# Optimization experiments

Hardware: AMD Instinct MI355X
Metric: run time of the kernel (lower is better)

The kernel has to match this reference:

```python
import jax, jax.numpy as jnp
import numpy as np

B, N, E_PER = 64, 1024, 32768
IN_DIM, HID, K = 128, 128, 64
EPS = 1e-15


def setup_inputs() -> dict:
    key = jax.random.key(0)
    ks = jax.random.split(key, 16)
    x = jax.random.normal(ks[0], (B * N, IN_DIM), jnp.float32)
    off = (jnp.arange(B, dtype=jnp.int32) * N)[:, None]
    src = (jax.random.randint(ks[1], (B, E_PER), 0, N, dtype=jnp.int32) + off).reshape(-1)
    dst = (jax.random.randint(ks[2], (B, E_PER), 0, N, dtype=jnp.int32) + off).reshape(-1)
    edge_index = jnp.stack([src, dst])
    batch = jnp.repeat(jnp.arange(B, dtype=jnp.int32), N)

    def lin(k, i, o):
        return (jax.random.normal(k, (i, o), jnp.float32) / np.sqrt(i)).astype(jnp.float32)

    params = dict(
        W1l=lin(ks[3], IN_DIM, HID), b1l=jnp.zeros((HID,), jnp.float32), W1r=lin(ks[4], IN_DIM, HID),
        W2l=lin(ks[5], HID, K), b2l=jnp.zeros((K,), jnp.float32), W2r=lin(ks[6], HID, K),
        Wm=lin(ks[7], K, K), bm=jnp.zeros((K,), jnp.float32),
        Wrel=lin(ks[8], HID, HID), Wroot=lin(ks[9], HID, HID), broot=jnp.zeros((HID,), jnp.float32),
        Wc1=lin(ks[10], HID * K, HID), bc1=jnp.zeros((HID,), jnp.float32),
        Wc2=lin(ks[11], HID, 1), bc2=jnp.zeros((1,), jnp.float32),
    )
    return dict(x=x, edge_index=edge_index, batch=batch, num_graphs=B, nodes_per_graph=N, **params)


def _sage(x, src, dst, Wl, bl, Wr, n):
    # PyG SAGEConv: lin_l(mean_{j in N(i)} x_j) + lin_r(x_i); lin_r has no bias.
    agg = jax.ops.segment_sum(x[src], dst, num_segments=n)
    deg = jax.ops.segment_sum(jnp.ones((src.shape[0],), x.dtype), dst, num_segments=n)
    agg = agg / jnp.maximum(deg, 1.0)[:, None]
    return agg @ Wl + bl + x @ Wr


def reference(x, edge_index, batch, num_graphs, nodes_per_graph,
              W1l, b1l, W1r, W2l, b2l, W2r, Wm, bm,
              Wrel, Wroot, broot, Wc1, bc1, Wc2, bc2):
    Bn, Nn = num_graphs, nodes_per_graph
    n_total = Bn * Nn
    src, dst = edge_index[0], edge_index[1]

    z = jax.nn.leaky_relu(_sage(x, src, dst, W1l, b1l, W1r, n_total), 0.01)
    s = jax.nn.leaky_relu(_sage(z, src, dst, W2l, b2l, W2r, n_total), 0.01)
    s = s @ Wm + bm

    # to_dense_batch (equal-size graphs -> mask all True) and to_dense_adj
    z = z.reshape(Bn, Nn, -1)                      # [B, N, HID]
    s = s.reshape(Bn, Nn, -1)                      # [B, N, K]
    a = jnp.zeros((Bn, Nn, Nn), x.dtype).at[src // Nn, src % Nn, dst % Nn].add(1.0)

    # dense_diff_pool
    s = jax.nn.softmax(s, axis=-1)
    pooled = jnp.einsum('bnk,bnf->bkf', s, z)      # [B, K, HID]
    adj_p = jnp.einsum('bnk,bnm,bml->bkl', s, a, s)  # [B, K, K]
    link_loss = jnp.sqrt(jnp.sum((a - jnp.einsum('bnk,bmk->bnm', s, s)) ** 2)) / a.size
    ent_loss = jnp.mean(jnp.sum(-s * jnp.log(s + EPS), axis=-1))

    # DenseSAGEConv: lin_rel(adj@x / deg) + lin_root(x)
    agg = jnp.matmul(adj_p, pooled) / jnp.maximum(adj_p.sum(-1, keepdims=True), 1.0)
    h = jax.nn.leaky_relu(agg @ Wrel + pooled @ Wroot + broot, 0.01)

    h = h.reshape(Bn, -1)                          # [B, K*HID]
    logits = (jax.nn.leaky_relu(h @ Wc1 + bc1, 0.01) @ Wc2 + bc2).squeeze(-1)
    return logits, link_loss + ent_loss
```

## Files before the change

### kernel.cpp

```cpp
#include <hip/hip_runtime.h>
#include <math.h>

#define BATCH 64
#define NPG 1024
#define NT (BATCH*NPG)
#define EPER 32768
#define ETOT (BATCH*EPER)

typedef __attribute__((ext_vector_type(4))) float f32x4;
typedef __attribute__((ext_vector_type(8))) short s16x8;

__device__ __forceinline__ float lky(float x){ return x > 0.f ? x : 0.01f*x; }
__device__ __forceinline__ unsigned short f2bf(float f){
    unsigned u = __float_as_uint(f);
    u = u + 0x7FFFu + ((u >> 16) & 1u);
    return (unsigned short)(u >> 16);
}
__device__ __forceinline__ float bf2f_lo(unsigned v){ return __uint_as_float(v << 16); }
__device__ __forceinline__ float bf2f_hi(unsigned v){ return __uint_as_float(v & 0xFFFF0000u); }

__global__ void k_castx(const float* __restrict__ in, unsigned short* __restrict__ out, int n4){
    int i = blockIdx.x*256 + threadIdx.x;
    if (i < n4){
        float4 v = ((const float4*)in)[i];
        ushort4 o = { f2bf(v.x), f2bf(v.y), f2bf(v.z), f2bf(v.w) };
        ((ushort4*)out)[i] = o;
    }
}

__global__ void k_wprep(const float* __restrict__ W1l, const float* __restrict__ W1r,
                        const float* __restrict__ W2l, const float* __restrict__ W2r,
                        unsigned short* __restrict__ wt){
    int i = blockIdx.x*256 + threadIdx.x;
    if (i < 16384){ int k = i >> 7, n = i & 127; wt[n*128 + k] = f2bf(W1l[i]); }
    else if (i < 32768){ int j = i - 16384; int k = j >> 7, n = j & 127; wt[16384 + n*128 + k] = f2bf(W1r[j]); }
    else if (i < 40960){ int j = i - 32768; int k = j >> 6, n = j & 63; wt[32768 + n*128 + k] = f2bf(W2l[j]); }
    else if (i < 49152){ int j = i - 40960; int k = j >> 6, n = j & 63; wt[40960 + n*128 + k] = f2bf(W2r[j]); }
}

__global__ void __launch_bounds__(1024) k_a2lds(const int* __restrict__ src, const int* __restrict__ dst,
                                                unsigned* __restrict__ acc_out){
    __shared__ unsigned nib[32768];
    __shared__ unsigned red[16];
    int b = blockIdx.x, pass = blockIdx.y, tid = threadIdx.x;
    for (int i = tid; i < 32768; i += 1024) nib[i] = 0;
    __syncthreads();
    int base = b*EPER;
    for (int i = tid; i < EPER; i += 1024){
        unsigned key = (((unsigned)src[base+i] & 1023u) << 10) | ((unsigned)dst[base+i] & 1023u);
        if ((int)(key >> 18) == pass)
            atomicAdd(&nib[(key & 0x3FFFFu) >> 3], 1u << ((key & 7u)*4u));
    }
    __syncthreads();
    unsigned local = 0;
    for (int i = tid; i < 32768; i += 1024){
        unsigned w = nib[i];
        if (w){
            #pragma unroll
            for (int q = 0; q < 8; q++){ unsigned c = (w >> (4*q)) & 15u; local += c*c; }
        }
    }
    for (int o = 32; o; o >>= 1) local += __shfl_xor(local, o);
    if ((tid & 63) == 0) red[tid >> 6] = local;
    __syncthreads();
    if (tid == 0){
        unsigned s = 0;
        for (int q = 0; q < 16; q++) s += red[q];
        atomicAdd(acc_out, s);
    }
}

__global__ void __launch_bounds__(1024) k_csr(const int* __restrict__ src, const int* __restrict__ dst,
                                              int* __restrict__ ipd, int* __restrict__ ips,
                                              unsigned short* __restrict__ lst_d,
                                              unsigned short* __restrict__ lst_s){
    __shared__ unsigned eds[EPER];
    __shared__ int cnt[1024];
    __shared__ int buf[1024];
    int g = blockIdx.x, which = blockIdx.y, tid = threadIdx.x;
    cnt[tid] = 0;
    __syncthreads();
    int base = g*EPER;
    for (int i = tid; i < EPER; i += 1024){
        unsigned s = (unsigned)src[base+i] & 1023u;
        unsigned d = (unsigned)dst[base+i] & 1023u;
        eds[i] = (s << 10) | d;
        atomicAdd(&cnt[which ? s : d], 1);
    }
    __syncthreads();
    int v = cnt[tid];
    int x = v;
    buf[tid] = x; __syncthreads();
    for (int off = 1; off < 1024; off <<= 1){
        int t = (tid >= off) ? buf[tid - off] : 0;
        __syncthreads();
        x += t; buf[tid] = x; __syncthreads();
    }
    int excl = x - v;
    int* ip = which ? ips : ipd;
    ip[g*1024 + tid] = base + excl;
    if (g == 0 && tid == 0) ip[NT] = ETOT;
    cnt[tid] = excl;
    __syncthreads();
    unsigned short* lst = which ? lst_s : lst_d;
    for (int i = tid; i < EPER; i += 1024){
        unsigned key = eds[i];
        unsigned d = key & 1023u, s = key >> 10;
        unsigned idx = which ? s : d;
        unsigned val = which ? d : s;
        int p = atomicAdd(&cnt[idx], 1);
        lst[base + p] = (unsigned short)val;
    }
}

template<int MODE, int TD>
__global__ void __launch_bounds__(1024) k_aggl(
        const unsigned short* __restrict__ X, const int* __restrict__ indptr,
        const unsigned short* __restrict__ lst,
        const unsigned short* __restrict__ R, const float* __restrict__ bias,
        unsigned short* __restrict__ out){
    __shared__ uint2 tab[1024*9];
    constexpr int PPG = (TD == 128) ? 8 : 4;
    int bid = blockIdx.x;
    int xcd = bid & 7, j = bid >> 3;
    int gi = j / PPG, part = j - gi*PPG;
    int graph = xcd + 8*gi;
    int fpart = part >> 1;
    int npart = part & 1;
    int foff = fpart*32;
    int nbase_loc = npart*512;
    int tid = threadIdx.x;
    int gb = graph*NPG;
    for (int i = tid; i < 8192; i += 1024){
        int row = i >> 3, q = i & 7;
        tab[row*9 + q] = *(const uint2*)&X[(size_t)(gb+row)*TD + foff + q*4];
    }
    __syncthreads();
    int g = tid & 7;
    for (int c = 0; c < 4; c++){
        int node = gb + nbase_loc + c*128 + (tid >> 3);
        int st = indptr[node], en = indptr[node+1];
        float a0 = 0.f, a1 = 0.f, a2 = 0.f, a3 = 0.f;
        int e = st;
        for (; e + 4 <= en; e += 4){
            int r0 = lst[e+0], r1 = lst[e+1], r2 = lst[e+2], r3 = lst[e+3];
            uint2 v0 = tab[r0*9 + g];
            uint2 v1 = tab[r1*9 + g];
            uint2 v2 = tab[r2*9 + g];
            uint2 v3 = tab[r3*9 + g];
            a0 += bf2f_lo(v0.x) + bf2f_lo(v1.x) + bf2f_lo(v2.x) + bf2f_lo(v3.x);
            a1 += bf2f_hi(v0.x) + bf2f_hi(v1.x) + bf2f_hi(v2.x) + bf2f_hi(v3.x);
            a2 += bf2f_lo(v0.y) + bf2f_lo(v1.y) + bf2f_lo(v2.y) + bf2f_lo(v3.y);
            a3 += bf2f_hi(v0.y) + bf2f_hi(v1.y) + bf2f_hi(v2.y) + bf2f_hi(v3.y);
        }
        for (; e < en; e++){
            uint2 v = tab[lst[e]*9 + g];
            a0 += bf2f_lo(v.x); a1 += bf2f_hi(v.x);
            a2 += bf2f_lo(v.y); a3 += bf2f_hi(v.y);
        }
        if (MODE >= 1){
            int dg = en - st;
            float inv = 1.f/(float)(dg > 1 ? dg : 1);
            a0 *= inv; a1 *= inv; a2 *= inv; a3 *= inv;
        }
        if (MODE == 2){
            uint2 r = *(const uint2*)&R[(size_t)node*TD + foff + 4*g];
            a0 = lky(a0 + bf2f_lo(r.x) + bias[foff + 4*g + 0]);
            a1 = lky(a1 + bf2f_hi(r.x) + bias[foff + 4*g + 1]);
            a2 = lky(a2 + bf2f_lo(r.y) + bias[foff + 4*g + 2]);
            a3 = lky(a3 + bf2f_hi(r.y) + bias[foff + 4*g + 3]);
        }
        uint2 pk;
        pk.x = (unsigned)f2bf(a0) | ((unsigned)f2bf(a1) << 16);
        pk.y = (unsigned)f2bf(a2) | ((unsigned)f2bf(a3) << 16);
        *(uint2*)&out[(size_t)node*TD + foff + 4*g] = pk;
    }
}

template<int N>
__global__ void __launch_bounds__(512) k_mfma2b(
        const unsigned short* __restrict__ Ah, const unsigned short* __restrict__ Wt1,
        const unsigned short* __restrict__ Wt2, unsigned short* __restrict__ C1,
        unsigned short* __restrict__ C2){
    __shared__ unsigned short ldsB[2*N*128];
    int tid = threadIdx.x;
    for (int i = tid; i < N*64; i += 512){
        int n = i >> 6, kk = i & 63;
        int swz = (n*256 + 4*kk) ^ ((n & 7) << 4);
        *(unsigned*)((char*)ldsB + swz)         = ((const unsigned*)Wt1)[i];
        *(unsigned*)((char*)ldsB + N*256 + swz) = ((const unsigned*)Wt2)[i];
    }
    __syncthreads();
    int wave = tid >> 6, l = tid & 63;
    int lr = l & 15, lg = l >> 4;
    constexpr int NF = N/16;
    int arow = blockIdx.x*128 + wave*16 + lr;
    f32x4 acc1[NF], acc2[NF];
    f32x4 zv = {0.f, 0.f, 0.f, 0.f};
    #pragma unroll
    for (int nf = 0; nf < NF; nf++){ acc1[nf] = zv; acc2[nf] = zv; }
    #pragma unroll
    for (int ks = 0; ks < 4; ks++){
        s16x8 af = *(const s16x8*)(Ah + (size_t)arow*128 + ks*32 + lg*8);
        #pragma unroll
        for (int nf = 0; nf < NF; nf++){
            int n = nf*16 + lr;
            int swz = (n*256 + ks*64 + lg*16) ^ ((n & 7) << 4);
            s16x8 b1 = *(const s16x8*)((const char*)ldsB + swz);
            s16x8 b2 = *(const s16x8*)((const char*)ldsB + N*256 + swz);
            acc1[nf] = __builtin_amdgcn_mfma_f32_16x16x32_bf16(af, b1, acc1[nf], 0, 0, 0);
            acc2[nf] = __builtin_amdgcn_mfma_f32_16x16x32_bf16(af, b2, acc2[nf], 0, 0, 0);
        }
    }
    int orow = blockIdx.x*128 + wave*16 + lg*4;
    #pragma unroll
    for (int nf = 0; nf < NF; nf++){
        int c = nf*16 + lr;
        #pragma unroll
        for (int j = 0; j < 4; j++){
            size_t idx = (size_t)(orow + j)*N + c;
            C1[idx] = f2bf(acc1[nf][j]);
            C2[idx] = f2bf(acc2[nf][j]);
        }
    }
}

__global__ void __launch_bounds__(256) k_gemm(
        const float* __restrict__ A1, const float* __restrict__ A2,
        const float* __restrict__ W1, const float* __restrict__ W2,
        const float* __restrict__ bias, void* __restrict__ C,
        int M, int Nn, int Kd, int dual, int act, int obf){
    __shared__ float sA1[16*68], sB1[16*68], sA2[16*68], sB2[16*68];
    int tid = threadIdx.x;
    int m0 = blockIdx.x*64, n0 = blockIdx.y*64;
    int tx = tid & 15, ty = tid >> 4;
    int lr = tid >> 2, lk = (tid & 3)*4;
    int wk = tid >> 4, wn = (tid & 15)*4;
    float acc[4][4] = {};
    for (int k0 = 0; k0 < Kd; k0 += 16){
        float4 a1 = *(const float4*)&A1[(size_t)(m0+lr)*Kd + k0 + lk];
        float4 w1 = *(const float4*)&W1[(size_t)(k0+wk)*Nn + n0 + wn];
        sA1[(lk+0)*68+lr] = a1.x; sA1[(lk+1)*68+lr] = a1.y;
        sA1[(lk+2)*68+lr] = a1.z; sA1[(lk+3)*68+lr] = a1.w;
        *(float4*)&sB1[wk*68+wn] = w1;
        if (dual){
            float4 a2 = *(const float4*)&A2[(size_t)(m0+lr)*Kd + k0 + lk];
            float4 w2 = *(const float4*)&W2[(size_t)(k0+wk)*Nn + n0 + wn];
            sA2[(lk+0)*68+lr] = a2.x; sA2[(lk+1)*68+lr] = a2.y;
            sA2[(lk+2)*68+lr] = a2.z; sA2[(lk+3)*68+lr] = a2.w;
            *(float4*)&sB2[wk*68+wn] = w2;
        }
        __syncthreads();
        #pragma unroll
        for (int kk = 0; kk < 16; kk++){
            float4 av = *(const float4*)&sA1[kk*68 + ty*4];
            float4 bv = *(const float4*)&sB1[kk*68 + tx*4];
            float a[4] = {av.x, av.y, av.z, av.w};
            float b[4] = {bv.x, bv.y, bv.z, bv.w};
            #pragma unroll
            for (int i = 0; i < 4; i++)
                #pragma unroll
                for (int j = 0; j < 4; j++) acc[i][j] += a[i]*b[j];
            if (dual){
                float4 av2 = *(const float4*)&sA2[kk*68 + ty*4];
                float4 bv2 = *(const float4*)&sB2[kk*68 + tx*4];
                float a2[4] = {av2.x, av2.y, av2.z, av2.w};
                float b2[4] = {bv2.x, bv2.y, bv2.z, bv2.w};
                #pragma unroll
                for (int i = 0; i < 4; i++)
                    #pragma unroll
                    for (int j = 0; j < 4; j++) acc[i][j] += a2[i]*b2[j];
            }
        }
        __syncthreads();
    }
    float bb[4] = {0.f, 0.f, 0.f, 0.f};
    if (bias){
        #pragma unroll
        for (int j = 0; j < 4; j++) bb[j] = bias[n0 + tx*4 + j];
    }
    #pragma unroll
    for (int i = 0; i < 4; i++){
        float v0 = acc[i][0]+bb[0], v1 = acc[i][1]+bb[1], v2 = acc[i][2]+bb[2], v3 = acc[i][3]+bb[3];
        if (act){ v0 = lky(v0); v1 = lky(v1); v2 = lky(v2); v3 = lky(v3); }
        size_t idx = (size_t)(m0 + ty*4 + i)*Nn + n0 + tx*4;
        if (obf){
            ushort4 o = { f2bf(v0), f2bf(v1), f2bf(v2), f2bf(v3) };
            *(ushort4*)&((unsigned short*)C)[idx] = o;
        } else {
            float4 o = { v0, v1, v2, v3 };
            *(float4*)&((float*)C)[idx] = o;
        }
    }
}

__global__ void __launch_bounds__(256) k_gemm_wm(
        const unsigned short* __restrict__ agg2h, const unsigned short* __restrict__ r2h,
        const float* __restrict__ b2l, const float* __restrict__ Wm,
        const float* __restrict__ bm,
        unsigned short* __restrict__ Sh, float* __restrict__ ent_acc){
    __shared__ float sA[16*68], sB[16*68];
    __shared__ float red[256];
    int tid = threadIdx.x;
    int m0 = blockIdx.x*64;
    int tx = tid & 15, ty = tid >> 4;
    int lr = tid >> 2, lk = (tid & 3)*4;
    int wk = tid >> 4, wn = (tid & 15)*4;
    float acc[4][4] = {};
    for (int k0 = 0; k0 < 64; k0 += 16){
        uint2 a = *(const uint2*)&agg2h[(size_t)(m0+lr)*64 + k0 + lk];
        uint2 r = *(const uint2*)&r2h[(size_t)(m0+lr)*64 + k0 + lk];
        sA[(lk+0)*68+lr] = lky(bf2f_lo(a.x) + bf2f_lo(r.x) + b2l[k0+lk+0]);
        sA[(lk+1)*68+lr] = lky(bf2f_hi(a.x) + bf2f_hi(r.x) + b2l[k0+lk+1]);
        sA[(lk+2)*68+lr] = lky(bf2f_lo(a.y) + bf2f_lo(r.y) + b2l[k0+lk+2]);
        sA[(lk+3)*68+lr] = lky(bf2f_hi(a.y) + bf2f_hi(r.y) + b2l[k0+lk+3]);
        *(float4*)&sB[wk*68+wn] = *(const float4*)&Wm[(size_t)(k0+wk)*64 + wn];
        __syncthreads();
        #pragma unroll
        for (int kk = 0; kk < 16; kk++){
            float4 av = *(const float4*)&sA[kk*68 + ty*4];
            float4 bv = *(const float4*)&sB[kk*68 + tx*4];
            float a4[4] = {av.x, av.y, av.z, av.w};
            float b4[4] = {bv.x, bv.y, bv.z, bv.w};
            #pragma unroll
            for (int i = 0; i < 4; i++)
                #pragma unroll
                for (int j = 0; j < 4; j++) acc[i][j] += a4[i]*b4[j];
        }
        __syncthreads();
    }
    float bb[4];
    #pragma unroll
    for (int j = 0; j < 4; j++) bb[j] = bm[tx*4 + j];
    float ent_local = 0.f;
    #pragma unroll
    for (int i = 0; i < 4; i++){
        float v[4];
        #pragma unroll
        for (int j = 0; j < 4; j++) v[j] = acc[i][j] + bb[j];
        float m = fmaxf(fmaxf(v[0], v[1]), fmaxf(v[2], v[3]));
        for (int o = 1; o < 16; o <<= 1) m = fmaxf(m, __shfl_xor(m, o));
        float e[4];
        float sm = 0.f;
        #pragma unroll
        for (int j = 0; j < 4; j++){ e[j] = __expf(v[j] - m); sm += e[j]; }
        for (int o = 1; o < 16; o <<= 1) sm += __shfl_xor(sm, o);
        float inv = 1.f/sm;
        float p[4];
        float w = 0.f;
        #pragma unroll
        for (int j = 0; j < 4; j++){
            p[j] = e[j]*inv;
            w += -p[j]*__logf(p[j] + 1e-15f);
        }
        for (int o = 1; o < 16; o <<= 1) w += __shfl_xor(w, o);
        if (tx == 0) ent_local += w;
        size_t idx = (size_t)(m0 + ty*4 + i)*64 + tx*4;
        ushort4 oh = { f2bf(p[0]), f2bf(p[1]), f2bf(p[2]), f2bf(p[3]) };
        *(ushort4*)&Sh[idx] = oh;
    }
    red[tid] = ent_local; __syncthreads();
    for (int o = 128; o; o >>= 1){ if (tid < o) red[tid] += red[tid+o]; __syncthreads(); }
    if (tid == 0) atomicAdd(ent_acc, red[0]);
}

__global__ void __launch_bounds__(1024) k_spmm(
        const unsigned short* __restrict__ Sh, const unsigned short* __restrict__ Zh,
        const unsigned short* __restrict__ Th,
        float* __restrict__ P, float* __restrict__ AP, float* __restrict__ GR,
        float* __restrict__ crossp, float* __restrict__ normgp){
    __shared__ unsigned short At[64*72];
    __shared__ unsigned short Bt[256*72];
    __shared__ float rtr[16], rsq[16];
    int b = blockIdx.x, tid = threadIdx.x;
    int w = tid >> 6, l = tid & 63;
    int lr = l & 15, lg = l >> 4;
    int mt = w & 3, ng = w >> 2;
    f32x4 acc[4];
    f32x4 zv = {0.f, 0.f, 0.f, 0.f};
    #pragma unroll
    for (int q = 0; q < 4; q++) acc[q] = zv;
    int gb = b*NPG;
    int sa_n = tid & 63, sa_c = (tid >> 6)*4;
    int sb_k = tid & 63, sb_g = tid >> 6;
    for (int n0 = 0; n0 < NPG; n0 += 64){
        ushort4 sv = *(const ushort4*)&Sh[(size_t)(gb+n0+sa_n)*64 + sa_c];
        At[(sa_c+0)*72 + sa_n] = sv.x;
        At[(sa_c+1)*72 + sa_n] = sv.y;
        At[(sa_c+2)*72 + sa_n] = sv.z;
        At[(sa_c+3)*72 + sa_n] = sv.w;
        {
            int R = gb + n0 + sb_k;
            const unsigned short* srcp;
            if (sb_g < 8)       srcp = &Zh[(size_t)R*128 + sb_g*16];
            else if (sb_g < 12) srcp = &Th[(size_t)R*64 + (sb_g-8)*16];
            else                srcp = &Sh[(size_t)R*64 + (sb_g-12)*16];
            ushort4 a0 = *(const ushort4*)(srcp);
            ushort4 a1 = *(const ushort4*)(srcp+4);
            ushort4 a2 = *(const ushort4*)(srcp+8);
            ushort4 a3 = *(const ushort4*)(srcp+12);
            int cb = sb_g*16;
            Bt[(cb+ 0)*72+sb_k]=a0.x; Bt[(cb+ 1)*72+sb_k]=a0.y; Bt[(cb+ 2)*72+sb_k]=a0.z; Bt[(cb+ 3)*72+sb_k]=a0.w;
            Bt[(cb+ 4)*72+sb_k]=a1.x; Bt[(cb+ 5)*72+sb_k]=a1.y; Bt[(cb+ 6)*72+sb_k]=a1.z; Bt[(cb+ 7)*72+sb_k]=a1.w;
            Bt[(cb+ 8)*72+sb_k]=a2.x; Bt[(cb+ 9)*72+sb_k]=a2.y; Bt[(cb+10)*72+sb_k]=a2.z; Bt[(cb+11)*72+sb_k]=a2.w;
            Bt[(cb+12)*72+sb_k]=a3.x; Bt[(cb+13)*72+sb_k]=a3.y; Bt[(cb+14)*72+sb_k]=a3.z; Bt[(cb+15)*72+sb_k]=a3.w;
        }
        __syncthreads();
        #pragma unroll
        for (int ks = 0; ks < 2; ks++){
            s16x8 af = *(const s16x8*)&At[(mt*16+lr)*72 + ks*32 + lg*8];
            #pragma unroll
            for (int q = 0; q < 4; q++){
                s16x8 bf = *(const s16x8*)&Bt[((ng*4+q)*16+lr)*72 + ks*32 + lg*8];
                acc[q] = __builtin_amdgcn_mfma_f32_16x16x32_bf16(af, bf, acc[q], 0, 0, 0);
            }
        }
        __syncthreads();
    }
    float tr = 0.f, sq = 0.f;
    #pragma unroll
    for (int q = 0; q < 4; q++){
        int col = (ng*4+q)*16 + lr;
        #pragma unroll
        for (int j = 0; j < 4; j++){
            int m = mt*16 + lg*4 + j;
            float v = acc[q][j];
            if (col < 128){
                P[((size_t)b*64+m)*128 + col] = v;
            } else if (col < 192){
                AP[((size_t)b*64+m)*64 + (col-128)] = v;
                if (col-128 == m) tr += v;
            } else {
                GR[((size_t)b*64+m)*64 + (col-192)] = v;
                sq += v*v;
            }
        }
    }
    for (int o = 32; o; o >>= 1){ tr += __shfl_xor(tr, o); sq += __shfl_xor(sq, o); }
    if (l == 0){ rtr[w] = tr; rsq[w] = sq; }
    __syncthreads();
    if (tid == 0){
        float str = 0.f, ssq = 0.f;
        for (int i = 0; i < 16; i++){ str += rtr[i]; ssq += rsq[i]; }
        atomicAdd(crossp, str);
        atomicAdd(normgp, ssq);
    }
}

__global__ void __launch_bounds__(256) k_heada(
        const float* __restrict__ AP, const float* __restrict__ P,
        float* __restrict__ aggout){
    __shared__ float sapT[64*65];
    __shared__ float sp[64*33];
    __shared__ float srs[64];
    int b = blockIdx.x, c0 = blockIdx.y*32;
    int tid = threadIdx.x;
    for (int i = tid; i < 4096; i += 256){
        int k = i >> 6, l = i & 63;
        sapT[l*65 + k] = AP[(size_t)b*4096 + i];
    }
    for (int i = tid; i < 2048; i += 256){
        int l = i >> 5, j = i & 31;
        sp[l*33 + j] = P[(size_t)b*8192 + l*128 + c0 + j];
    }
    __syncthreads();
    if (tid < 64){
        float s = 0.f;
        for (int l = 0; l < 64; l++) s += sapT[l*65 + tid];
        srs[tid] = fmaxf(s, 1.f);
    }
    __syncthreads();
    int k = tid & 63, jg = (tid >> 6)*8;
    float acc[8] = {};
    for (int l = 0; l < 64; l++){
        float a = sapT[l*65 + k];
        #pragma unroll
        for (int j = 0; j < 8; j++) acc[j] += a*sp[l*33 + jg + j];
    }
    float inv = 1.f/srs[k];
    #pragma unroll
    for (int j = 0; j < 8; j++)
        aggout[(size_t)b*8192 + k*128 + c0 + jg + j] = acc[j]*inv;
}

__global__ void __launch_bounds__(256) k_head2(
        const float* __restrict__ hbuf, const float* __restrict__ Wc1,
        float* __restrict__ hcacc){
    __shared__ float sh[512];
    __shared__ float sred[256];
    int b = blockIdx.x >> 4, ch = blockIdx.x & 15;
    int tid = threadIdx.x;
    for (int i = tid; i < 512; i += 256) sh[i] = hbuf[(size_t)b*8192 + ch*512 + i];
    __syncthreads();
    int j = tid & 127, half = tid >> 7;
    float acc = 0.f;
    const float* W = Wc1 + (size_t)(ch*512 + half*256)*128;
    const float* hh = sh + half*256;
    for (int r = 0; r < 256; r++) acc += hh[r]*W[(size_t)r*128 + j];
    sred[tid] = acc; __syncthreads();
    if (tid < 128) atomicAdd(&hcacc[(size_t)b*128 + tid], sred[tid] + sred[tid+128]);
}

__global__ void k_head3(const float* __restrict__ hcacc, const float* __restrict__ bc1,
                        const float* __restrict__ Wc2, const float* __restrict__ bc2,
                        float* __restrict__ out){
    int b = blockIdx.x, t = threadIdx.x;
    float hc = lky(hcacc[(size_t)b*128 + t] + bc1[t]);
    float p = hc*Wc2[t];
    for (int o = 32; o; o >>= 1) p += __shfl_xor(p, o);
    __shared__ float r2[2];
    if ((t & 63) == 0) r2[t >> 6] = p;
    __syncthreads();
    if (t == 0) out[b] = r2[0] + r2[1] + bc2[0];
}

__global__ void k_finalize(const unsigned int* __restrict__ a2,
                           const float* __restrict__ cross,
                           const float* __restrict__ normg,
                           const float* __restrict__ ent,
                           float* __restrict__ out){
    float ss = (float)(*a2) - 2.f*(*cross) + (*normg);
    if (ss < 0.f) ss = 0.f;
    float link = sqrtf(ss) / 67108864.f;
    out[64] = link + (*ent)/(float)NT;
}

extern "C" void kernel_launch(void* const* d_in, const int* in_sizes, int n_in,
                              void* d_out, int out_size, void* d_ws, size_t ws_size,
                              hipStream_t stream){
    const float* x    = (const float*)d_in[0];
    const int*   ei   = (const int*)d_in[1];
    const int*   src  = ei;
    const int*   dst  = ei + ETOT;
    const float* W1l  = (const float*)d_in[5];
    const float* b1l  = (const float*)d_in[6];
    const float* W1r  = (const float*)d_in[7];
    const float* W2l  = (const float*)d_in[8];
    const float* b2l  = (const float*)d_in[9];
    const float* W2r  = (const float*)d_in[10];
    const float* Wm   = (const float*)d_in[11];
    const float* bm   = (const float*)d_in[12];
    const float* Wrel = (const float*)d_in[13];
    const float* Wroot= (const float*)d_in[14];
    const float* broot= (const float*)d_in[15];
    const float* Wc1  = (const float*)d_in[16];
    const float* bc1  = (const float*)d_in[17];
    const float* Wc2  = (const float*)d_in[18];
    const float* bc2  = (const float*)d_in[19];
    float* out = (float*)d_out;

    char* w = (char*)d_ws;
    size_t off = 0;
    auto take = [&](size_t bytes)->void*{
        void* p = w + off; off = (off + bytes + 255) & ~(size_t)255; return p;
    };
    const size_t MB = 1024*1024;
    float* hcacc  = (float*)take((size_t)BATCH*128*4);
    float* accb   = (float*)take(64);
    size_t zero_small = off;
    unsigned short* wt = (unsigned short*)take((size_t)49152*2);
    float* pooled = (float*)take((size_t)BATCH*64*128*4);
    float* adjp   = (float*)take((size_t)BATCH*64*64*4);
    float* gram   = (float*)take((size_t)BATCH*64*64*4);
    int*   ipd   = (int*)take((size_t)(NT+1)*4);
    int*   ips   = (int*)take((size_t)(NT+1)*4);
    unsigned short* lst_d = (unsigned short*)take((size_t)ETOT*2);
    unsigned short* lst_s = (unsigned short*)take((size_t)ETOT*2);
    char*  regA  = (char*)take(16*MB);
    char*  regB  = (char*)take(16*MB);
    char*  regC  = (char*)take(16*MB);
    char*  regD  = (char*)take(16*MB);
    char*  regE  = (char*)take(16*MB);
    float* hbuf  = (float*)take((size_t)BATCH*8192*4);
    float* aggo  = (float*)take((size_t)BATCH*8192*4);

    unsigned short* y1h   = (unsigned short*)regB;
    unsigned short* th    = (unsigned short*)regB;
    unsigned short* r1h   = (unsigned short*)regC;
    unsigned short* y2h   = (unsigned short*)regC;
    unsigned short* s2h   = (unsigned short*)(regC + 8*MB);
    unsigned short* r2h   = (unsigned short*)regD;
    unsigned short* xh    = (unsigned short*)regE;
    unsigned short* zh    = (unsigned short*)regE;
    unsigned short* agg2h = (unsigned short*)regA;

    float* crossp = accb + 0;
    float* normgp = accb + 1;
    float* entp   = accb + 2;
    unsigned int* a2p = (unsigned int*)(accb + 3);

    hipMemsetAsync(d_ws, 0, zero_small, stream);

    k_wprep<<<192, 256, 0, stream>>>(W1l, W1r, W2l, W2r, wt);
    k_castx<<<NT*128/4/256, 256, 0, stream>>>(x, xh, NT*128/4);

    k_a2lds<<<dim3(BATCH, 4), 1024, 0, stream>>>(src, dst, a2p);

    k_csr<<<dim3(BATCH, 2), 1024, 0, stream>>>(src, dst, ipd, ips, lst_d, lst_s);

    k_mfma2b<128><<<NT/128, 512, 0, stream>>>(xh, wt, wt + 16384, y1h, r1h);
    k_aggl<2,128><<<512, 1024, 0, stream>>>(y1h, ipd, lst_d, r1h, b1l, zh);

    k_mfma2b<64><<<NT/128, 512, 0, stream>>>(zh, wt + 32768, wt + 40960, y2h, r2h);
    k_aggl<1,64><<<256, 1024, 0, stream>>>(y2h, ipd, lst_d, nullptr, nullptr, agg2h);
    k_gemm_wm<<<NT/64, 256, 0, stream>>>(agg2h, r2h, b2l, Wm, bm, s2h, entp);

    k_aggl<0,64><<<256, 1024, 0, stream>>>(s2h, ips, lst_s, nullptr, nullptr, th);

    k_spmm<<<BATCH, 1024, 0, stream>>>(s2h, zh, th, pooled, adjp, gram, crossp, normgp);

    k_heada<<<dim3(BATCH, 4), 256, 0, stream>>>(adjp, pooled, aggo);
    k_gemm<<<dim3(BATCH*64/64, 2), 256, 0, stream>>>(aggo, pooled, Wrel, Wroot, broot, hbuf, BATCH*64, 128, 128, 1, 1, 0);
    k_head2<<<BATCH*16, 256, 0, stream>>>(hbuf, Wc1, hcacc);
    k_head3<<<BATCH, 128, 0, stream>>>(hcacc, bc1, Wc2, bc2, out);
    k_finalize<<<1, 1, 0, stream>>>(a2p, crossp, normgp, entp, out);
}
```

Measured before the change: 286.2 us.

## Split k_spmm over node range into 4 partial blocks with separate reduction kernel

The per-graph dense product (pooled, adjp, gram) used to run on only 64 blocks, one per graph. It now splits each graph's 1024-node reduction into 4 chunks, launching 256 blocks with an XCD-aware graph mapping, and writes fp32 partials to a scratch buffer. A new reduction kernel sums the four partials, writes the outputs and computes the trace and squared-norm atomics. This raises occupancy on a 256-CU GPU, at the cost of an extra launch and about 16 MB of partial-buffer traffic.

```diff
diff --git a/kernel.cpp b/kernel.cpp
--- a/kernel.cpp
+++ b/kernel.cpp
@@ -366,13 +366,14 @@
 
 __global__ void __launch_bounds__(1024) k_spmm(
         const unsigned short* __restrict__ Sh, const unsigned short* __restrict__ Zh,
-        const unsigned short* __restrict__ Th,
-        float* __restrict__ P, float* __restrict__ AP, float* __restrict__ GR,
-        float* __restrict__ crossp, float* __restrict__ normgp){
+        const unsigned short* __restrict__ Th, float* __restrict__ pbuf){
     __shared__ unsigned short At[64*72];
     __shared__ unsigned short Bt[256*72];
-    __shared__ float rtr[16], rsq[16];
-    int b = blockIdx.x, tid = threadIdx.x;
+    int bid = blockIdx.x;
+    int xcd = bid & 7, j = bid >> 3;
+    int graph = xcd + 8*(j & 7);
+    int kp = j >> 3;
+    int tid = threadIdx.x;
     int w = tid >> 6, l = tid & 63;
     int lr = l & 15, lg = l >> 4;
     int mt = w & 3, ng = w >> 2;
@@ -380,10 +381,10 @@
     f32x4 zv = {0.f, 0.f, 0.f, 0.f};
     #pragma unroll
     for (int q = 0; q < 4; q++) acc[q] = zv;
-    int gb = b*NPG;
+    int gb = graph*NPG;
     int sa_n = tid & 63, sa_c = (tid >> 6)*4;
     int sb_k = tid & 63, sb_g = tid >> 6;
-    for (int n0 = 0; n0 < NPG; n0 += 64){
+    for (int n0 = kp*256; n0 < kp*256 + 256; n0 += 64){
         ushort4 sv = *(const ushort4*)&Sh[(size_t)(gb+n0+sa_n)*64 + sa_c];
         At[(sa_c+0)*72 + sa_n] = sv.x;
         At[(sa_c+1)*72 + sa_n] = sv.y;
@@ -417,33 +418,45 @@
         }
         __syncthreads();
     }
-    float tr = 0.f, sq = 0.f;
+    float* pb = pbuf + ((size_t)graph*4 + kp)*16384;
     #pragma unroll
     for (int q = 0; q < 4; q++){
         int col = (ng*4+q)*16 + lr;
         #pragma unroll
-        for (int j = 0; j < 4; j++){
-            int m = mt*16 + lg*4 + j;
-            float v = acc[q][j];
-            if (col < 128){
-                P[((size_t)b*64+m)*128 + col] = v;
-            } else if (col < 192){
-                AP[((size_t)b*64+m)*64 + (col-128)] = v;
-                if (col-128 == m) tr += v;
-            } else {
-                GR[((size_t)b*64+m)*64 + (col-192)] = v;
-                sq += v*v;
-            }
-        }
+        for (int j2 = 0; j2 < 4; j2++){
+            int m = mt*16 + lg*4 + j2;
+            pb[m*256 + col] = acc[q][j2];
+        }
+    }
+}
+
+__global__ void k_spmmred(const float* __restrict__ pbuf,
+                          float* __restrict__ P, float* __restrict__ AP,
+                          float* __restrict__ GR,
+                          float* __restrict__ crossp, float* __restrict__ normgp){
+    int i = blockIdx.x*256 + threadIdx.x;
+    int g = i >> 14;
+    int r = i & 16383;
+    int m = r >> 8, col = r & 255;
+    const float* pb = pbuf + (size_t)g*65536 + r;
+    float v = pb[0] + pb[16384] + pb[32768] + pb[49152];
+    float tr = 0.f, sq = 0.f;
+    if (col < 128){
+        P[((size_t)g*64 + m)*128 + col] = v;
+    } else if (col < 192){
+        AP[((size_t)g*64 + m)*64 + (col-128)] = v;
+        if (col-128 == m) tr = v;
+    } else {
+        GR[((size_t)g*64 + m)*64 + (col-192)] = v;
+        sq = v*v;
     }
     for (int o = 32; o; o >>= 1){ tr += __shfl_xor(tr, o); sq += __shfl_xor(sq, o); }
-    if (l == 0){ rtr[w] = tr; rsq[w] = sq; }
-    __syncthreads();
-    if (tid == 0){
-        float str = 0.f, ssq = 0.f;
-        for (int i = 0; i < 16; i++){ str += rtr[i]; ssq += rsq[i]; }
-        atomicAdd(crossp, str);
-        atomicAdd(normgp, ssq);
+    __shared__ float rt[4], rs[4];
+    if ((threadIdx.x & 63) == 0){ rt[threadIdx.x >> 6] = tr; rs[threadIdx.x >> 6] = sq; }
+    __syncthreads();
+    if (threadIdx.x == 0){
+        atomicAdd(crossp, rt[0]+rt[1]+rt[2]+rt[3]);
+        atomicAdd(normgp, rs[0]+rs[1]+rs[2]+rs[3]);
     }
 }
 
@@ -580,6 +593,7 @@
     unsigned short* y2h   = (unsigned short*)regC;
     unsigned short* s2h   = (unsigned short*)(regC + 8*MB);
     unsigned short* r2h   = (unsigned short*)regD;
+    float*          pbuf  = (float*)regD;
     unsigned short* xh    = (unsigned short*)regE;
     unsigned short* zh    = (unsigned short*)regE;
     unsigned short* agg2h = (unsigned short*)regA;
@@ -607,7 +621,8 @@
 
     k_aggl<0,64><<<256, 1024, 0, stream>>>(s2h, ips, lst_s, nullptr, nullptr, th);
 
-    k_spmm<<<BATCH, 1024, 0, stream>>>(s2h, zh, th, pooled, adjp, gram, crossp, normgp);
+    k_spmm<<<256, 1024, 0, stream>>>(s2h, zh, th, pbuf);
+    k_spmmred<<<4096, 256, 0, stream>>>(pbuf, pooled, adjp, gram, crossp, normgp);
 
     k_heada<<<dim3(BATCH, 4), 256, 0, stream>>>(adjp, pooled, aggo);
     k_gemm<<<dim3(BATCH*64/64, 2), 256, 0, stream>>>(aggo, pooled, Wrel, Wroot, broot, hbuf, BATCH*64, 128, 128, 1, 1, 0);
```

After: 368.0 us. +28.6%, slower.
